# Kernel optimization log

Hardware: AMD Instinct MI355X
Metric: run time of the kernel (lower is better)

## Reference

```python
import math
import jax, jax.numpy as jnp
import numpy as np


def _gelu(x):
    return jax.nn.gelu(x, approximate=False)


def _bilinear_sample(feat, gx, gy):
    """grid_sample, mode=bilinear, padding=border, align_corners=True.
    feat: [B,C,H,W]; gx,gy: [B,M] in [-1,1]. Returns [B,M,C]."""
    B, C, H, W = feat.shape
    x = jnp.clip((gx + 1.0) * 0.5 * (W - 1), 0.0, W - 1)
    y = jnp.clip((gy + 1.0) * 0.5 * (H - 1), 0.0, H - 1)
    x0 = jnp.floor(x); y0 = jnp.floor(y)
    wx = (x - x0)[..., None]; wy = (y - y0)[..., None]
    x0i = x0.astype(jnp.int32); y0i = y0.astype(jnp.int32)
    x1i = jnp.minimum(x0i + 1, W - 1); y1i = jnp.minimum(y0i + 1, H - 1)
    ft = jnp.transpose(feat, (0, 2, 3, 1))  # [B,H,W,C]
    gather = jax.vmap(lambda f, yi, xi: f[yi, xi])
    v00 = gather(ft, y0i, x0i); v01 = gather(ft, y0i, x1i)
    v10 = gather(ft, y1i, x0i); v11 = gather(ft, y1i, x1i)
    return (v00 * (1 - wx) * (1 - wy) + v01 * wx * (1 - wy)
            + v10 * (1 - wx) * wy + v11 * wx * wy)


def _layernorm(x, w, b, eps=1e-5):
    m = jnp.mean(x, -1, keepdims=True)
    v = jnp.var(x, -1, keepdims=True)
    return (x - m) / jnp.sqrt(v + eps) * w + b


def _gfb(h, f_next, ph_w, ph_b, gate, w1, b1, w2, b2, ln_w, ln_b):
    g = jax.nn.sigmoid(gate)
    fused = f_next + g * (h @ ph_w + ph_b)
    fused = _gelu(fused @ w1 + b1) @ w2 + b2
    return _layernorm(fused, ln_w, ln_b)


def _forward(img, feat_s8, feat_s16, coarse_flow, query_coords,
             pp_w1, pp_b1, pp_w2, pp_b2, p8_w, p8_b, p16_w, p16_b,
             f1_ph_w, f1_ph_b, f1_gate, f1_w1, f1_b1, f1_w2, f1_b2, f1_ln_w, f1_ln_b,
             f2_ph_w, f2_ph_b, f2_gate, f2_w1, f2_b1, f2_w2, f2_b2, f2_ln_w, f2_ln_b,
             h_w1, h_b1, h_w2, h_b2, h_w3, h_b3):
    B, _, H, W = img.shape
    N = query_coords.shape[1]
    k = 5; half = k // 2
    H8, W8 = coarse_flow.shape[2], coarse_flow.shape[3]
    # normalized grid at query points (x,y)
    gx = 2.0 * query_coords[..., 0] / (W - 1) - 1.0
    gy = 2.0 * query_coords[..., 1] / (H - 1) - 1.0
    coarse_q = _bilinear_sample(coarse_flow, gx, gy)  # [B,N,2]
    coarse_q = coarse_q * jnp.array([W / W8, H / H8], coarse_q.dtype)
    # local k x k RGB patches
    offs = jnp.arange(-half, half + 1, dtype=img.dtype)
    oy, ox = jnp.meshgrid(offs, offs, indexing='ij')
    og = jnp.stack([ox.reshape(-1), oy.reshape(-1)], -1)  # [k*k,2]
    ce = query_coords[:, :, None, :] + og                # [B,N,kk,2]
    pgx = (2.0 * ce[..., 0] / (W - 1) - 1.0).reshape(B, -1)
    pgy = (2.0 * ce[..., 1] / (H - 1) - 1.0).reshape(B, -1)
    patches = _bilinear_sample(img, pgx, pgy).reshape(B, N, k * k * 3)
    f_local = _gelu(patches @ pp_w1 + pp_b1) @ pp_w2 + pp_b2
    f8 = _bilinear_sample(feat_s8, gx, gy) @ p8_w + p8_b
    f16 = _bilinear_sample(feat_s16, gx, gy) @ p16_w + p16_b
    D = f_local.shape[-1]
    h = f_local.reshape(B * N, D)
    h = _gfb(h, f8.reshape(B * N, D), f1_ph_w, f1_ph_b, f1_gate,
             f1_w1, f1_b1, f1_w2, f1_b2, f1_ln_w, f1_ln_b)
    h = _gfb(h, f16.reshape(B * N, D), f2_ph_w, f2_ph_b, f2_gate,
             f2_w1, f2_b1, f2_w2, f2_b2, f2_ln_w, f2_ln_b)
    # relative-in-cell coords + sinusoidal PE (6 bands)
    qx = query_coords[..., 0] / (W / W8)
    qy = query_coords[..., 1] / (H / H8)
    local = jnp.stack([(qx - jnp.round(qx)) * 2.0, (qy - jnp.round(qy)) * 2.0], -1)
    freqs = (2.0 ** jnp.arange(6, dtype=local.dtype)) * math.pi
    xf = local[..., None] * freqs                        # [B,N,2,6]
    enc = jnp.concatenate([jnp.sin(xf), jnp.cos(xf)], -1).reshape(B, N, 24)
    pe = jnp.concatenate([local, enc], -1).reshape(B * N, 26)
    coarse_flat = coarse_q.reshape(B * N, 2)
    mi = jnp.concatenate([h, pe, coarse_flat], -1)       # [B*N, 156]
    delta = _gelu(_gelu(mi @ h_w1 + h_b1) @ h_w2 + h_b2) @ h_w3 + h_b3
    return (coarse_flat + delta).reshape(B, N, 2)


def setup_inputs() -> dict:
    key = jax.random.key(0)
    ks = jax.random.split(key, 40)
    B, H, W = 2, 384, 512
    H8, W8, H16, W16 = 48, 64, 24, 32
    N, D, k = 65536, 128, 5
    pf = 3 * k * k
    def p(i, shape):
        return jax.random.normal(ks[i], shape, jnp.float32) * 0.05
    return {
        'img': jax.random.uniform(ks[0], (B, 3, H, W), jnp.float32),
        'feat_s8': jax.random.normal(ks[1], (B, D, H8, W8), jnp.float32),
        'feat_s16': jax.random.normal(ks[2], (B, D, H16, W16), jnp.float32),
        'coarse_flow': jax.random.normal(ks[3], (B, 2, H8, W8), jnp.float32),
        'query_coords': jax.random.uniform(ks[4], (B, N, 2), jnp.float32)
                        * jnp.array([W - 1.0, H - 1.0], jnp.float32),
        'pp_w1': p(5, (pf, D)), 'pp_b1': p(6, (D,)),
        'pp_w2': p(7, (D, D)), 'pp_b2': p(8, (D,)),
        'p8_w': p(9, (D, D)), 'p8_b': p(10, (D,)),
        'p16_w': p(11, (D, D)), 'p16_b': p(12, (D,)),
        'f1_ph_w': p(13, (D, D)), 'f1_ph_b': p(14, (D,)), 'f1_gate': p(15, (D,)),
        'f1_w1': p(16, (D, 2 * D)), 'f1_b1': p(17, (2 * D,)),
        'f1_w2': p(18, (2 * D, D)), 'f1_b2': p(19, (D,)),
        'f1_ln_w': 1.0 + p(20, (D,)), 'f1_ln_b': p(21, (D,)),
        'f2_ph_w': p(22, (D, D)), 'f2_ph_b': p(23, (D,)), 'f2_gate': p(24, (D,)),
        'f2_w1': p(25, (D, 2 * D)), 'f2_b1': p(26, (2 * D,)),
        'f2_w2': p(27, (2 * D, D)), 'f2_b2': p(28, (D,)),
        'f2_ln_w': 1.0 + p(29, (D,)), 'f2_ln_b': p(30, (D,)),
        'h_w1': p(31, (D + 26 + 2, 128)), 'h_b1': p(32, (128,)),
        'h_w2': p(33, (128, 64)), 'h_b2': p(34, (64,)),
        'h_w3': p(35, (64, 2)), 'h_b3': p(36, (2,)),
    }


def reference(img, feat_s8, feat_s16, coarse_flow, query_coords,
              pp_w1, pp_b1, pp_w2, pp_b2, p8_w, p8_b, p16_w, p16_b,
              f1_ph_w, f1_ph_b, f1_gate, f1_w1, f1_b1, f1_w2, f1_b2, f1_ln_w, f1_ln_b,
              f2_ph_w, f2_ph_b, f2_gate, f2_w1, f2_b1, f2_w2, f2_b2, f2_ln_w, f2_ln_b,
              h_w1, h_b1, h_w2, h_b2, h_w3, h_b3):
    return _forward(img, feat_s8, feat_s16, coarse_flow, query_coords,
                    pp_w1, pp_b1, pp_w2, pp_b2, p8_w, p8_b, p16_w, p16_b,
                    f1_ph_w, f1_ph_b, f1_gate, f1_w1, f1_b1, f1_w2, f1_b2, f1_ln_w, f1_ln_b,
                    f2_ph_w, f2_ph_b, f2_gate, f2_w1, f2_b1, f2_w2, f2_b2, f2_ln_w, f2_ln_b,
                    h_w1, h_b1, h_w2, h_b2, h_w3, h_b3)
```

## Files before the change

kernel.cpp:

```cpp
#include <hip/hip_runtime.h>
#include <math.h>

#define NT 512
#define MB 64
#define MTOT 131072
#define IMG_H 384
#define IMG_W 512
#define H8 48
#define W8 64
#define H16 24
#define W16 32

#define SAB 128
#define SPE 40

typedef _Float16 half8_t __attribute__((ext_vector_type(8)));
typedef _Float16 half4_t __attribute__((ext_vector_type(4)));
typedef float f32x4_t __attribute__((ext_vector_type(4)));
typedef unsigned short u16;

#define SWZ(r, gi) ((gi) ^ ((r) & 7))

#define PW_PP1    0
#define PW_MEGA1  12288
#define PW_S8     77824
#define PW_MEGA2  110592
#define PW_S15    176128
#define PW_HW1    208896
#define PW_HW2    229376
#define PW_END    237568
#define FT8_OFF   PW_END
#define FT8_CNT   (2*H8*W8*128)
#define FT16_OFF  (FT8_OFF + FT8_CNT)
#define FT16_CNT  (2*H16*W16*128)
#define F32_OFF   (FT16_OFF + FT16_CNT)
#define PEG_OFF   (F32_OFF + 2*164608)
#define PEG_CNT   (2048*MB*SPE)
#define CBG_OFF   (PEG_OFF + PEG_CNT)

__device__ __forceinline__ u16 tohalf(float v) {
  return __builtin_bit_cast(u16, (_Float16)v);
}
__device__ __forceinline__ float geluf(float x) {
  float x2 = x * x;
  float t = x * fmaf(x2, 0.0713548162726f, 1.5957691216057308f);
  float e = __expf(-t);
  return x * __builtin_amdgcn_rcpf(1.0f + e);
}

__device__ __forceinline__ float bilin_plane(const float* __restrict__ plane,
                                             int Wd, int Hd, float x, float y) {
  x = fminf(fmaxf(x, 0.f), (float)(Wd - 1));
  y = fminf(fmaxf(y, 0.f), (float)(Hd - 1));
  float x0f = floorf(x), y0f = floorf(y);
  int x0 = (int)x0f, y0 = (int)y0f;
  int x1 = min(x0 + 1, Wd - 1), y1 = min(y0 + 1, Hd - 1);
  float wx = x - x0f, wy = y - y0f;
  const float* r0 = plane + y0 * Wd;
  const float* r1 = plane + y1 * Wd;
  float v00 = r0[x0], v01 = r0[x1], v10 = r1[x0], v11 = r1[x1];
  float top = v00 + wx * (v01 - v00);
  float bot = v10 + wx * (v11 - v10);
  return top + wy * (bot - top);
}

__device__ __forceinline__ void featSample(const u16* __restrict__ ft, int Wd, int Hd,
                                           float x, float y, u16* dstRow,
                                           int i16, int giS) {
  x = fminf(fmaxf(x, 0.f), (float)(Wd - 1));
  y = fminf(fmaxf(y, 0.f), (float)(Hd - 1));
  float x0f = floorf(x), y0f = floorf(y);
  int x0 = (int)x0f, y0 = (int)y0f;
  int x1 = min(x0 + 1, Wd - 1), y1 = min(y0 + 1, Hd - 1);
  _Float16 wx = (_Float16)(x - x0f), wy = (_Float16)(y - y0f);
  half8_t v00 = *reinterpret_cast<const half8_t*>(ft + (y0 * Wd + x0) * 128 + i16 * 8);
  half8_t v01 = *reinterpret_cast<const half8_t*>(ft + (y0 * Wd + x1) * 128 + i16 * 8);
  half8_t v10 = *reinterpret_cast<const half8_t*>(ft + (y1 * Wd + x0) * 128 + i16 * 8);
  half8_t v11 = *reinterpret_cast<const half8_t*>(ft + (y1 * Wd + x1) * 128 + i16 * 8);
  half8_t top = v00 + wx * (v01 - v00);
  half8_t bot = v10 + wx * (v11 - v10);
  half8_t r = top + wy * (bot - top);
  *reinterpret_cast<half8_t*>(dstRow + giS * 8) = r;
}

template <int KT, int SPLITKT, int ACT, int SWB = 1, int NWAVES = 8>
__device__ __forceinline__ void mmv(
    const u16* __restrict__ wpk,
    const u16* aA, const u16* aB, int strB,
    const float* __restrict__ bias,
    u16* ob) {
  const int tid = threadIdx.x;
  const int lane = tid & 63;
  const int w = tid >> 6;
  const int l15 = lane & 15;
  const int g = lane >> 4;
  if (NWAVES == 8 || w < NWAVES) {
    f32x4_t acc[4];
#pragma unroll
    for (int mt = 0; mt < 4; ++mt) acc[mt] = (f32x4_t){0.f, 0.f, 0.f, 0.f};
    __builtin_amdgcn_s_setprio(1);
#pragma unroll
    for (int kt = 0; kt < KT; ++kt) {
      half8_t af[4];
#pragma unroll
      for (int mt = 0; mt < 4; ++mt) {
        const int row = mt * 16 + l15;
        const u16* p;
        if (kt < SPLITKT) {
          p = aA + row * 128 + SWZ(row, kt * 4 + g) * 8;
        } else if (SWB) {
          p = aB + row * 128 + SWZ(row, (kt - SPLITKT) * 4 + g) * 8;
        } else {
          p = aB + row * strB + (kt - SPLITKT) * 32 + g * 8;
        }
        af[mt] = *reinterpret_cast<const half8_t*>(p);
      }
      half8_t bf = *reinterpret_cast<const half8_t*>(wpk + ((w * KT + kt) * 64 + lane) * 8);
#pragma unroll
      for (int mt = 0; mt < 4; ++mt)
        acc[mt] = __builtin_amdgcn_mfma_f32_16x16x32_f16(bf, af[mt], acc[mt], 0, 0, 0);
    }
    __builtin_amdgcn_s_setprio(0);
    const int c0 = (w << 4) + (g << 2);
    f32x4_t bv = *reinterpret_cast<const f32x4_t*>(bias + c0);
#pragma unroll
    for (int mt = 0; mt < 4; ++mt) {
      const int row = (mt << 4) + l15;
      half4_t hv;
#pragma unroll
      for (int r = 0; r < 4; ++r) {
        float v = acc[mt][r] + bv[r];
        if (ACT == 1) v = geluf(v);
        hv[r] = (_Float16)v;
      }
      const int e = row * 128 + (c0 ^ ((row & 7) << 3));
      *reinterpret_cast<half4_t*>(ob + e) = hv;
    }
  }
}

__device__ __forceinline__ void lnorm(const u16* src, u16* dst,
                                      const float* __restrict__ lw,
                                      const float* __restrict__ lb) {
  const int tid = threadIdx.x;
  int q = tid >> 3, s = tid & 7;
  float xs[16];
  float sum = 0.f, sum2 = 0.f;
#pragma unroll
  for (int c8 = 0; c8 < 2; ++c8) {
    const int gi = SWZ(q, 2 * s + c8);
    half8_t v = *reinterpret_cast<const half8_t*>(src + q * 128 + gi * 8);
#pragma unroll
    for (int j = 0; j < 8; ++j) {
      float x = (float)v[j];
      xs[c8 * 8 + j] = x; sum += x; sum2 += x * x;
    }
  }
  sum += __shfl_xor(sum, 1); sum2 += __shfl_xor(sum2, 1);
  sum += __shfl_xor(sum, 2); sum2 += __shfl_xor(sum2, 2);
  sum += __shfl_xor(sum, 4); sum2 += __shfl_xor(sum2, 4);
  float mean = sum * 0.0078125f;
  float var = sum2 * 0.0078125f - mean * mean;
  float rstd = rsqrtf(var + 1e-5f);
#pragma unroll
  for (int c8 = 0; c8 < 2; ++c8) {
    half8_t r;
#pragma unroll
    for (int j = 0; j < 8; ++j) {
      int c = s * 16 + c8 * 8 + j;
      r[j] = (_Float16)((xs[c8 * 8 + j] - mean) * rstd * lw[c] + lb[c]);
    }
    const int gi = SWZ(q, 2 * s + c8);
    *reinterpret_cast<half8_t*>(dst + q * 128 + gi * 8) = r;
  }
}

struct PrepArgs {
  const float *f1_ph_w, *f1_gate, *f2_ph_w, *f2_gate;
  const float *p8_w, *p16_w, *f1_w1, *f2_w1;
  const float *p8_b, *f1_ph_b, *p16_b, *f2_ph_b, *f2_b1;
  const float *feat8, *feat16;
  float *T1, *WAtop, *WBtop, *WBbot, *bvec1, *bB;
  u16 *ft8, *ft16;
};

__global__ void prepA(PrepArgs a) {
  const int blk = blockIdx.x;
  const int tid = threadIdx.x;
  if (blk < 2056) {
    const int o = tid >> 2, ks = tid & 3;
    float acc = 0.f;
    if (blk < 2048) {
      const int sec = blk >> 9;
      const int oid = (blk & 511) * 64 + o;
      const int r = oid >> 8, n = oid & 255;
#pragma unroll 8
      for (int i = 0; i < 32; ++i) {
        const int m = ks * 32 + i;
        if (sec == 0) {
          float sig = __builtin_amdgcn_rcpf(1.f + __expf(-a.f1_gate[m]));
          acc += sig * a.f1_ph_w[r * 128 + m] * a.f1_w1[m * 256 + n];
        } else if (sec == 1) {
          acc += a.p8_w[r * 128 + m] * a.f1_w1[m * 256 + n];
        } else if (sec == 2) {
          acc += a.p16_w[r * 128 + m] * a.f2_w1[m * 256 + n];
        } else {
          float sig = __builtin_amdgcn_rcpf(1.f + __expf(-a.f2_gate[m]));
          acc += sig * a.f2_ph_w[r * 128 + m] * a.f2_w1[m * 256 + n];
        }
      }
      acc += __shfl_xor(acc, 1);
      acc += __shfl_xor(acc, 2);
      if (ks == 0) {
        float* dst = (sec == 0) ? a.T1 : (sec == 1) ? a.WAtop
                     : (sec == 2) ? a.WBtop : a.WBbot;
        dst[oid] = acc;
      }
    } else {
      const int oid = (blk - 2048) * 64 + o;
#pragma unroll 8
      for (int i = 0; i < 32; ++i) {
        const int m = ks * 32 + i;
        if (oid < 256) {
          float sig = __builtin_amdgcn_rcpf(1.f + __expf(-a.f1_gate[m]));
          acc += (a.p8_b[m] + sig * a.f1_ph_b[m]) * a.f1_w1[m * 256 + oid];
        } else {
          float sig = __builtin_amdgcn_rcpf(1.f + __expf(-a.f2_gate[m]));
          acc += (a.p16_b[m] + sig * a.f2_ph_b[m]) * a.f2_w1[m * 256 + (oid - 256)];
        }
      }
      acc += __shfl_xor(acc, 1);
      acc += __shfl_xor(acc, 2);
      if (ks == 0) {
        if (oid < 256) a.bvec1[oid] = acc;
        else a.bB[oid - 256] = a.f2_b1[oid - 256] + acc;
      }
    }
  } else {
    const int tot8 = 2 * 128 * H8 * W8;
    const int i = (blk - 2056) * 256 + tid;
    if (i < tot8) {
      int x = i % W8;
      int t = i / W8;
      int y = t % H8; t /= H8;
      int c = t % 128;
      int b = t / 128;
      a.ft8[((b * H8 + y) * W8 + x) * 128 + c] = tohalf(a.feat8[i]);
    } else {
      int i2 = i - tot8;
      int x = i2 % W16;
      int t = i2 / W16;
      int y = t % H16; t /= H16;
      int c = t % 128;
      int b = t / 128;
      a.ft16[((b * H16 + y) * W16 + x) * 128 + c] = tohalf(a.feat16[i2]);
    }
  }
}

__global__ void prepB(const float* __restrict__ pp_w2, const float* __restrict__ T1,
                      const float* __restrict__ pp_b2, const float* __restrict__ f1_b1,
                      const float* __restrict__ bvec1,
                      float* __restrict__ WAbot, float* __restrict__ bA) {
  const int blk = blockIdx.x;
  const int tid = threadIdx.x;
  const int o = tid >> 2, ks = tid & 3;
  float acc = 0.f;
  if (blk < 512) {
    const int oid = blk * 64 + o;
    const int k = oid >> 8, n = oid & 255;
#pragma unroll 8
    for (int i = 0; i < 32; ++i) {
      const int r = ks * 32 + i;
      acc += pp_w2[k * 128 + r] * T1[r * 256 + n];
    }
    acc += __shfl_xor(acc, 1);
    acc += __shfl_xor(acc, 2);
    if (ks == 0) WAbot[oid] = acc;
  } else {
    const int n = (blk - 512) * 64 + o;
#pragma unroll 8
    for (int i = 0; i < 32; ++i) {
      const int r = ks * 32 + i;
      acc += pp_b2[r] * T1[r * 256 + n];
    }
    acc += __shfl_xor(acc, 1);
    acc += __shfl_xor(acc, 2);
    if (ks == 0) bA[n] = f1_b1[n] + bvec1[n] + acc;
  }
}

struct PackArgs {
  const float *pp_w1, *f1_w2, *f2_w2, *h_w1, *h_w2;
  const float *WAtop, *WAbot, *WBtop, *WBbot;
  u16* dst;
};

__global__ void pack_weights(PackArgs a) {
  const int KTs[7]   = {3, 8, 8, 8, 8, 5, 4};
  const int Ks[7]    = {75, 256, 256, 256, 256, 156, 128};
  const int bases[8] = {0, 12288, 77824, 110592, 176128, 208896, 229376, 237568};
  int stride = gridDim.x * blockDim.x;
  for (int i = blockIdx.x * blockDim.x + threadIdx.x; i < PW_END; i += stride) {
    int s = 0;
    while (i >= bases[s + 1]) ++s;
    int rem = i - bases[s];
    int e = rem & 511, lane = e >> 3, j = e & 7;
    int ntkt = rem >> 9;
    int kt = ntkt % KTs[s], nt = ntkt / KTs[s];
    int k = kt * 32 + ((lane >> 4) << 3) + j;
    int col = (nt << 4) + (lane & 15);
    float v = 0.f;
    if (k < Ks[s]) {
      switch (s) {
        case 0: v = a.pp_w1[k * 128 + col]; break;
        case 1: v = (k < 128) ? a.WAtop[k * 256 + col]
                              : a.WAbot[(k - 128) * 256 + col]; break;
        case 2: v = a.f1_w2[k * 128 + col]; break;
        case 3: v = (k < 128) ? a.WBtop[k * 256 + col]
                              : a.WBbot[(k - 128) * 256 + col]; break;
        case 4: v = a.f2_w2[k * 128 + col]; break;
        case 5: v = a.h_w1[k * 128 + col]; break;
        case 6: v = a.h_w2[k * 64 + col]; break;
      }
    }
    a.dst[i] = tohalf(v);
  }
}

struct KParams {
  const float *img, *coarse_flow, *qc;
  const u16 *wpk, *ft8, *ft16;
  const float *bA, *bB;
  u16* peg;
  float* cbg;
  const float *pp_b1;
  const float *f1_b2, *f1_ln_w, *f1_ln_b;
  const float *f2_b2, *f2_ln_w, *f2_ln_b;
  const float *h_b1, *h_b2, *h_w3, *h_b3;
  float* out;
};

__global__ __launch_bounds__(NT, 2) void ifd_mfma(KParams P) {
  __shared__ __align__(16) u16 smem[4 * MB * SAB];
  u16* ab0 = smem;
  u16* ab1 = smem + MB * SAB;
  u16* tb  = smem + 2 * MB * SAB;
  u16* hb  = smem + 3 * MB * SAB;

  const int tid = threadIdx.x;
  const int m0 = blockIdx.x * MB;
  u16* pegB = P.peg + blockIdx.x * (MB * SPE);
  float* cbgB = P.cbg + blockIdx.x * (MB * 2);

  {
    const int q = tid >> 3, sub = tid & 7;
    const int m = m0 + q, b = m >> 16;
    const float qx = P.qc[2 * m], qy = P.qc[2 * m + 1];
    const float* imgb = P.img + b * 3 * (IMG_H * IMG_W);
#pragma unroll
    for (int j = 0; j < 12; ++j) {
      const int c = sub * 12 + j;
      u16 val = 0;
      if (c < 75) {
        int p = c / 3, ch = c - p * 3;
        int iy = p / 5, ix = p - iy * 5;
        val = tohalf(bilin_plane(imgb + ch * (IMG_H * IMG_W), IMG_W, IMG_H,
                                 qx + (float)(ix - 2), qy + (float)(iy - 2)));
      }
      ab0[q * 128 + (c ^ ((q & 7) << 3))] = val;
    }
  }
  if (tid < 128) {
    const int q = tid >> 1, dim = tid & 1;
    const int m = m0 + q;
    const float qv = P.qc[2 * m + dim];
    const float q8 = qv * 0.125f;
    const float loc = (q8 - rintf(q8)) * 2.f;
    pegB[q * SPE + dim] = tohalf(loc);
    const float th = loc * 3.14159265358979323846f;
    float s = __sinf(th), c = __cosf(th);
    const int base = q * SPE + 2 + dim * 12;
#pragma unroll
    for (int bnd = 0; bnd < 6; ++bnd) {
      pegB[base + bnd] = tohalf(s);
      pegB[base + 6 + bnd] = tohalf(c);
      float s2 = 2.f * s * c;
      c = fmaf(-2.f * s, s, 1.f);
      s = s2;
    }
  } else if (tid < 256) {
    const int t2 = tid - 128, q = t2 >> 1, o = t2 & 1;
    const int m = m0 + q, b = m >> 16;
    const float qx = P.qc[2 * m], qy = P.qc[2 * m + 1];
    const float x8 = qx * (63.f / 511.f), y8 = qy * (47.f / 383.f);
    const float cv = 8.f * bilin_plane(P.coarse_flow + (b * 2 + o) * (H8 * W8),
                                       W8, H8, x8, y8);
    pegB[q * SPE + 26 + o] = tohalf(cv);
    cbgB[q * 2 + o] = cv;
  } else if (tid < 384) {
    const int t2 = tid - 256, q = t2 >> 1, pr = t2 & 1;
    *reinterpret_cast<unsigned int*>(pegB + q * SPE + 28 + 2 * pr) = 0u;
  }
  __syncthreads();

  mmv<3, 3, 1>(P.wpk + PW_PP1, ab0, ab0, 128, P.pp_b1, ab1);
  for (int i = tid; i < MB * 16; i += NT) {
    int q = i >> 4, i16 = i & 15;
    int m = m0 + q, b = m >> 16;
    float x = P.qc[2 * m] * (63.f / 511.f), y = P.qc[2 * m + 1] * (47.f / 383.f);
    featSample(P.ft8 + b * (H8 * W8 * 128), W8, H8, x, y, hb + q * 128,
               i16, SWZ(q, i16));
  }
  __syncthreads();

  mmv<8, 4, 1>(P.wpk + PW_MEGA1, hb, ab1, 128, P.bA, ab0);
  mmv<8, 4, 1>(P.wpk + PW_MEGA1 + 32768, hb, ab1, 128, P.bA + 128, tb);
  __syncthreads();

  mmv<8, 4, 0>(P.wpk + PW_S8, ab0, tb, 128, P.f1_b2, ab1);
  __syncthreads();

  lnorm(ab1, hb, P.f1_ln_w, P.f1_ln_b);
  for (int i = tid; i < MB * 16; i += NT) {
    int q = i >> 4, i16 = i & 15;
    int m = m0 + q, b = m >> 16;
    float x = P.qc[2 * m] * (31.f / 511.f), y = P.qc[2 * m + 1] * (23.f / 383.f);
    featSample(P.ft16 + b * (H16 * W16 * 128), W16, H16, x, y, ab0 + q * 128,
               i16, SWZ(q, i16));
  }
  __syncthreads();

  mmv<8, 4, 1>(P.wpk + PW_MEGA2, ab0, hb, 128, P.bB, ab1);
  mmv<8, 4, 1>(P.wpk + PW_MEGA2 + 32768, ab0, hb, 128, P.bB + 128, tb);
  __syncthreads();

  mmv<8, 4, 0>(P.wpk + PW_S15, ab1, tb, 128, P.f2_b2, ab0);
  __syncthreads();

  lnorm(ab0, hb, P.f2_ln_w, P.f2_ln_b);
  __syncthreads();

  mmv<5, 4, 1, 0>(P.wpk + PW_HW1, hb, pegB, SPE, P.h_b1, ab1);
  __syncthreads();

  mmv<4, 4, 1, 1, 4>(P.wpk + PW_HW2, ab1, ab1, 128, P.h_b2, ab0);
  __syncthreads();

  if (tid < 2 * MB) {
    int q = tid >> 1, o = tid & 1;
    float acc = P.h_b3[o];
    const u16* rp = ab0 + q * 128;
#pragma unroll
    for (int c8 = 0; c8 < 8; ++c8) {
      half8_t v = *reinterpret_cast<const half8_t*>(rp + SWZ(q, c8) * 8);
#pragma unroll
      for (int j = 0; j < 8; ++j) acc += (float)v[j] * P.h_w3[(c8 * 8 + j) * 2 + o];
    }
    P.out[(m0 + q) * 2 + o] = cbgB[q * 2 + o] + acc;
  }
}

extern "C" void kernel_launch(void* const* d_in, const int* in_sizes, int n_in,
                              void* d_out, int out_size, void* d_ws, size_t ws_size,
                              hipStream_t stream) {
  u16* wp = (u16*)d_ws;
  float* fbase = (float*)(wp + F32_OFF);
  float* T1    = fbase;
  float* WAtop = fbase + 32768;
  float* WAbot = fbase + 65536;
  float* WBtop = fbase + 98304;
  float* WBbot = fbase + 131072;
  float* bvec1 = fbase + 163840;
  float* bA    = fbase + 164096;
  float* bB    = fbase + 164352;
  u16* peg = wp + PEG_OFF;
  float* cbg = (float*)(wp + CBG_OFF);

  PrepArgs pra;
  pra.f1_ph_w = (const float*)d_in[13];
  pra.f1_gate = (const float*)d_in[15];
  pra.f2_ph_w = (const float*)d_in[22];
  pra.f2_gate = (const float*)d_in[24];
  pra.p8_w = (const float*)d_in[9];
  pra.p16_w = (const float*)d_in[11];
  pra.f1_w1 = (const float*)d_in[16];
  pra.f2_w1 = (const float*)d_in[25];
  pra.p8_b = (const float*)d_in[10];
  pra.f1_ph_b = (const float*)d_in[14];
  pra.p16_b = (const float*)d_in[12];
  pra.f2_ph_b = (const float*)d_in[23];
  pra.f2_b1 = (const float*)d_in[26];
  pra.feat8 = (const float*)d_in[1];
  pra.feat16 = (const float*)d_in[2];
  pra.T1 = T1; pra.WAtop = WAtop; pra.WBtop = WBtop; pra.WBbot = WBbot;
  pra.bvec1 = bvec1; pra.bB = bB;
  pra.ft8 = wp + FT8_OFF; pra.ft16 = wp + FT16_OFF;
  prepA<<<2056 + 3840, 256, 0, stream>>>(pra);

  prepB<<<516, 256, 0, stream>>>((const float*)d_in[7], T1, (const float*)d_in[8],
                                 (const float*)d_in[17], bvec1, WAbot, bA);

  PackArgs pa;
  pa.pp_w1 = (const float*)d_in[5];
  pa.f1_w2 = (const float*)d_in[18];
  pa.f2_w2 = (const float*)d_in[27];
  pa.h_w1  = (const float*)d_in[31];
  pa.h_w2  = (const float*)d_in[33];
  pa.WAtop = WAtop; pa.WAbot = WAbot; pa.WBtop = WBtop; pa.WBbot = WBbot;
  pa.dst = wp;
  pack_weights<<<464, 256, 0, stream>>>(pa);

  KParams P;
  P.img = (const float*)d_in[0];
  P.coarse_flow = (const float*)d_in[3];
  P.qc = (const float*)d_in[4];
  P.wpk = wp; P.ft8 = wp + FT8_OFF; P.ft16 = wp + FT16_OFF;
  P.bA = bA; P.bB = bB;
  P.peg = peg; P.cbg = cbg;
  P.pp_b1 = (const float*)d_in[6];
  P.f1_b2 = (const float*)d_in[19];
  P.f1_ln_w = (const float*)d_in[20]; P.f1_ln_b = (const float*)d_in[21];
  P.f2_b2 = (const float*)d_in[28];
  P.f2_ln_w = (const float*)d_in[29]; P.f2_ln_b = (const float*)d_in[30];
  P.h_b1 = (const float*)d_in[32]; P.h_b2 = (const float*)d_in[34];
  P.h_w3 = (const float*)d_in[35]; P.h_b3 = (const float*)d_in[36];
  P.out = (float*)d_out;

  ifd_mfma<<<MTOT / MB, NT, 0, stream>>>(P);
}
```

Measured before the change: 196.5 us.

## Merge three weight-prep kernels into one prep_all launch with reassociated products

Replaces the prepA, prepB and pack_weights launches with a single prep_all kernel. Each block builds one row of the folded weight matrix in LDS, multiplies it by W1 and writes the packed fp16 MFMA layout directly, so the fp32 intermediates T1/WA/WB are no longer stored and reloaded. The pp_w2·f1_ph_w product is reassociated so it is computed per row before multiplying by W1. This removes two launches and their global round trips. The cost is serial 128-long dot products per thread with low parallelism in the row blocks.

```diff
diff --git a/kernel.cpp b/kernel.cpp
--- a/kernel.cpp
+++ b/kernel.cpp
@@ -34,7 +34,7 @@
 #define FT16_OFF  (FT8_OFF + FT8_CNT)
 #define FT16_CNT  (2*H16*W16*128)
 #define F32_OFF   (FT16_OFF + FT16_CNT)
-#define PEG_OFF   (F32_OFF + 2*164608)
+#define PEG_OFF   (F32_OFF + 2*512)
 #define PEG_CNT   (2048*MB*SPE)
 #define CBG_OFF   (PEG_OFF + PEG_CNT)
 
@@ -175,70 +175,97 @@
   }
 }
 
-struct PrepArgs {
-  const float *f1_ph_w, *f1_gate, *f2_ph_w, *f2_gate;
-  const float *p8_w, *p16_w, *f1_w1, *f2_w1;
-  const float *p8_b, *f1_ph_b, *p16_b, *f2_ph_b, *f2_b1;
+struct PrepAllArgs {
+  const float *pp_w1, *pp_w2, *p8_w, *p16_w, *f1_ph_w, *f1_gate, *f1_w1, *f1_w2;
+  const float *f2_ph_w, *f2_gate, *f2_w1, *f2_w2, *h_w1, *h_w2;
+  const float *p8_b, *f1_ph_b, *pp_b2, *f1_b1, *p16_b, *f2_ph_b, *f2_b1;
   const float *feat8, *feat16;
-  float *T1, *WAtop, *WBtop, *WBbot, *bvec1, *bB;
+  u16 *dst;
+  float *bA, *bB;
   u16 *ft8, *ft16;
 };
 
-__global__ void prepA(PrepArgs a) {
+__global__ void prep_all(PrepAllArgs a) {
+  __shared__ float lds[256];
   const int blk = blockIdx.x;
   const int tid = threadIdx.x;
-  if (blk < 2056) {
-    const int o = tid >> 2, ks = tid & 3;
-    float acc = 0.f;
-    if (blk < 2048) {
-      const int sec = blk >> 9;
-      const int oid = (blk & 511) * 64 + o;
-      const int r = oid >> 8, n = oid & 255;
-#pragma unroll 8
-      for (int i = 0; i < 32; ++i) {
-        const int m = ks * 32 + i;
-        if (sec == 0) {
-          float sig = __builtin_amdgcn_rcpf(1.f + __expf(-a.f1_gate[m]));
-          acc += sig * a.f1_ph_w[r * 128 + m] * a.f1_w1[m * 256 + n];
-        } else if (sec == 1) {
-          acc += a.p8_w[r * 128 + m] * a.f1_w1[m * 256 + n];
-        } else if (sec == 2) {
-          acc += a.p16_w[r * 128 + m] * a.f2_w1[m * 256 + n];
-        } else {
-          float sig = __builtin_amdgcn_rcpf(1.f + __expf(-a.f2_gate[m]));
-          acc += sig * a.f2_ph_w[r * 128 + m] * a.f2_w1[m * 256 + n];
+  if (blk < 512) {
+    const int sec = blk >> 8;
+    const int k = blk & 255;
+    float* Arow = lds;
+    if (sec == 0) {
+      if (k < 128) {
+        if (tid < 128) Arow[tid] = a.p8_w[k * 128 + tid];
+      } else {
+        float* prow = lds + 128;
+        if (tid < 128) prow[tid] = a.pp_w2[(k - 128) * 128 + tid];
+        __syncthreads();
+        if (tid < 128) {
+          float sig = __builtin_amdgcn_rcpf(1.f + __expf(-a.f1_gate[tid]));
+          float acc = 0.f;
+          for (int r = 0; r < 128; ++r) acc += prow[r] * a.f1_ph_w[r * 128 + tid];
+          Arow[tid] = acc * sig;
         }
       }
-      acc += __shfl_xor(acc, 1);
-      acc += __shfl_xor(acc, 2);
-      if (ks == 0) {
-        float* dst = (sec == 0) ? a.T1 : (sec == 1) ? a.WAtop
-                     : (sec == 2) ? a.WBtop : a.WBbot;
-        dst[oid] = acc;
-      }
     } else {
-      const int oid = (blk - 2048) * 64 + o;
-#pragma unroll 8
-      for (int i = 0; i < 32; ++i) {
-        const int m = ks * 32 + i;
-        if (oid < 256) {
-          float sig = __builtin_amdgcn_rcpf(1.f + __expf(-a.f1_gate[m]));
-          acc += (a.p8_b[m] + sig * a.f1_ph_b[m]) * a.f1_w1[m * 256 + oid];
-        } else {
-          float sig = __builtin_amdgcn_rcpf(1.f + __expf(-a.f2_gate[m]));
-          acc += (a.p16_b[m] + sig * a.f2_ph_b[m]) * a.f2_w1[m * 256 + (oid - 256)];
+      if (k < 128) {
+        if (tid < 128) Arow[tid] = a.p16_w[k * 128 + tid];
+      } else {
+        if (tid < 128) {
+          float sig = __builtin_amdgcn_rcpf(1.f + __expf(-a.f2_gate[tid]));
+          Arow[tid] = a.f2_ph_w[(k - 128) * 128 + tid] * sig;
         }
       }
-      acc += __shfl_xor(acc, 1);
-      acc += __shfl_xor(acc, 2);
-      if (ks == 0) {
-        if (oid < 256) a.bvec1[oid] = acc;
-        else a.bB[oid - 256] = a.f2_b1[oid - 256] + acc;
-      }
-    }
+    }
+    __syncthreads();
+    const float* W1 = (sec == 0) ? a.f1_w1 : a.f2_w1;
+    float acc = 0.f;
+    for (int m = 0; m < 128; ++m) acc += Arow[m] * W1[m * 256 + tid];
+    const int kt = k >> 5, hi = (k >> 3) & 3, j = k & 7;
+    const int nt = tid >> 4, lo = tid & 15;
+    const int base = (sec == 0) ? PW_MEGA1 : PW_MEGA2;
+    a.dst[base + (((nt * 8 + kt) * 64 + hi * 16 + lo) << 3) + j] = tohalf(acc);
+  } else if (blk == 512) {
+    float* u = lds;
+    if (tid < 128) {
+      float sig = __builtin_amdgcn_rcpf(1.f + __expf(-a.f1_gate[tid]));
+      float acc = 0.f;
+      for (int r = 0; r < 128; ++r) acc += a.pp_b2[r] * a.f1_ph_w[r * 128 + tid];
+      u[tid] = a.p8_b[tid] + sig * a.f1_ph_b[tid] + sig * acc;
+    }
+    __syncthreads();
+    float acc = a.f1_b1[tid];
+    for (int m = 0; m < 128; ++m) acc += u[m] * a.f1_w1[m * 256 + tid];
+    a.bA[tid] = acc;
+  } else if (blk == 513) {
+    float acc = a.f2_b1[tid];
+    for (int m = 0; m < 128; ++m) {
+      float sig = __builtin_amdgcn_rcpf(1.f + __expf(-a.f2_gate[m]));
+      acc += (a.p16_b[m] + sig * a.f2_ph_b[m]) * a.f2_w1[m * 256 + tid];
+    }
+    a.bB[tid] = acc;
+  } else if (blk < 930) {
+    const int vi = (blk - 514) * 256 + tid;
+    const int vb[6] = {0, 12288, 45056, 77824, 98304, 106496};
+    const int KTs[5] = {3, 8, 8, 5, 4};
+    const int Ks[5]  = {75, 256, 256, 156, 128};
+    const int Ns[5]  = {128, 128, 128, 128, 64};
+    const int pw[5]  = {PW_PP1, PW_S8, PW_S15, PW_HW1, PW_HW2};
+    int s = 0;
+    while (vi >= vb[s + 1]) ++s;
+    const int rem = vi - vb[s];
+    const int e = rem & 511, lane = e >> 3, j = e & 7;
+    const int ntkt = rem >> 9;
+    const int kt = ntkt % KTs[s], nt = ntkt / KTs[s];
+    const int k = kt * 32 + ((lane >> 4) << 3) + j;
+    const int col = (nt << 4) + (lane & 15);
+    const float* src = (s == 0) ? a.pp_w1 : (s == 1) ? a.f1_w2
+                     : (s == 2) ? a.f2_w2 : (s == 3) ? a.h_w1 : a.h_w2;
+    float v = (k < Ks[s]) ? src[k * Ns[s] + col] : 0.f;
+    a.dst[pw[s] + rem] = tohalf(v);
   } else {
     const int tot8 = 2 * 128 * H8 * W8;
-    const int i = (blk - 2056) * 256 + tid;
+    const int i = (blk - 930) * 256 + tid;
     if (i < tot8) {
       int x = i % W8;
       int t = i / W8;
@@ -258,76 +285,6 @@
   }
 }
 
-__global__ void prepB(const float* __restrict__ pp_w2, const float* __restrict__ T1,
-                      const float* __restrict__ pp_b2, const float* __restrict__ f1_b1,
-                      const float* __restrict__ bvec1,
-                      float* __restrict__ WAbot, float* __restrict__ bA) {
-  const int blk = blockIdx.x;
-  const int tid = threadIdx.x;
-  const int o = tid >> 2, ks = tid & 3;
-  float acc = 0.f;
-  if (blk < 512) {
-    const int oid = blk * 64 + o;
-    const int k = oid >> 8, n = oid & 255;
-#pragma unroll 8
-    for (int i = 0; i < 32; ++i) {
-      const int r = ks * 32 + i;
-      acc += pp_w2[k * 128 + r] * T1[r * 256 + n];
-    }
-    acc += __shfl_xor(acc, 1);
-    acc += __shfl_xor(acc, 2);
-    if (ks == 0) WAbot[oid] = acc;
-  } else {
-    const int n = (blk - 512) * 64 + o;
-#pragma unroll 8
-    for (int i = 0; i < 32; ++i) {
-      const int r = ks * 32 + i;
-      acc += pp_b2[r] * T1[r * 256 + n];
-    }
-    acc += __shfl_xor(acc, 1);
-    acc += __shfl_xor(acc, 2);
-    if (ks == 0) bA[n] = f1_b1[n] + bvec1[n] + acc;
-  }
-}
-
-struct PackArgs {
-  const float *pp_w1, *f1_w2, *f2_w2, *h_w1, *h_w2;
-  const float *WAtop, *WAbot, *WBtop, *WBbot;
-  u16* dst;
-};
-
-__global__ void pack_weights(PackArgs a) {
-  const int KTs[7]   = {3, 8, 8, 8, 8, 5, 4};
-  const int Ks[7]    = {75, 256, 256, 256, 256, 156, 128};
-  const int bases[8] = {0, 12288, 77824, 110592, 176128, 208896, 229376, 237568};
-  int stride = gridDim.x * blockDim.x;
-  for (int i = blockIdx.x * blockDim.x + threadIdx.x; i < PW_END; i += stride) {
-    int s = 0;
-    while (i >= bases[s + 1]) ++s;
-    int rem = i - bases[s];
-    int e = rem & 511, lane = e >> 3, j = e & 7;
-    int ntkt = rem >> 9;
-    int kt = ntkt % KTs[s], nt = ntkt / KTs[s];
-    int k = kt * 32 + ((lane >> 4) << 3) + j;
-    int col = (nt << 4) + (lane & 15);
-    float v = 0.f;
-    if (k < Ks[s]) {
-      switch (s) {
-        case 0: v = a.pp_w1[k * 128 + col]; break;
-        case 1: v = (k < 128) ? a.WAtop[k * 256 + col]
-                              : a.WAbot[(k - 128) * 256 + col]; break;
-        case 2: v = a.f1_w2[k * 128 + col]; break;
-        case 3: v = (k < 128) ? a.WBtop[k * 256 + col]
-                              : a.WBbot[(k - 128) * 256 + col]; break;
-        case 4: v = a.f2_w2[k * 128 + col]; break;
-        case 5: v = a.h_w1[k * 128 + col]; break;
-        case 6: v = a.h_w2[k * 64 + col]; break;
-      }
-    }
-    a.dst[i] = tohalf(v);
-  }
-}
-
 struct KParams {
   const float *img, *coarse_flow, *qc;
   const u16 *wpk, *ft8, *ft16;
@@ -466,50 +423,40 @@
                               hipStream_t stream) {
   u16* wp = (u16*)d_ws;
   float* fbase = (float*)(wp + F32_OFF);
-  float* T1    = fbase;
-  float* WAtop = fbase + 32768;
-  float* WAbot = fbase + 65536;
-  float* WBtop = fbase + 98304;
-  float* WBbot = fbase + 131072;
-  float* bvec1 = fbase + 163840;
-  float* bA    = fbase + 164096;
-  float* bB    = fbase + 164352;
+  float* bA = fbase;
+  float* bB = fbase + 256;
   u16* peg = wp + PEG_OFF;
   float* cbg = (float*)(wp + CBG_OFF);
 
-  PrepArgs pra;
+  PrepAllArgs pra;
+  pra.pp_w1 = (const float*)d_in[5];
+  pra.pp_w2 = (const float*)d_in[7];
+  pra.p8_w  = (const float*)d_in[9];
+  pra.p16_w = (const float*)d_in[11];
   pra.f1_ph_w = (const float*)d_in[13];
   pra.f1_gate = (const float*)d_in[15];
+  pra.f1_w1 = (const float*)d_in[16];
+  pra.f1_w2 = (const float*)d_in[18];
   pra.f2_ph_w = (const float*)d_in[22];
   pra.f2_gate = (const float*)d_in[24];
-  pra.p8_w = (const float*)d_in[9];
-  pra.p16_w = (const float*)d_in[11];
-  pra.f1_w1 = (const float*)d_in[16];
   pra.f2_w1 = (const float*)d_in[25];
-  pra.p8_b = (const float*)d_in[10];
+  pra.f2_w2 = (const float*)d_in[27];
+  pra.h_w1  = (const float*)d_in[31];
+  pra.h_w2  = (const float*)d_in[33];
+  pra.p8_b  = (const float*)d_in[10];
   pra.f1_ph_b = (const float*)d_in[14];
+  pra.pp_b2 = (const float*)d_in[8];
+  pra.f1_b1 = (const float*)d_in[17];
   pra.p16_b = (const float*)d_in[12];
   pra.f2_ph_b = (const float*)d_in[23];
   pra.f2_b1 = (const float*)d_in[26];
   pra.feat8 = (const float*)d_in[1];
   pra.feat16 = (const float*)d_in[2];
-  pra.T1 = T1; pra.WAtop = WAtop; pra.WBtop = WBtop; pra.WBbot = WBbot;
-  pra.bvec1 = bvec1; pra.bB = bB;
-  pra.ft8 = wp + FT8_OFF; pra.ft16 = wp + FT16_OFF;
-  prepA<<<2056 + 3840, 256, 0, stream>>>(pra);
-
-  prepB<<<516, 256, 0, stream>>>((const float*)d_in[7], T1, (const float*)d_in[8],
-                                 (const float*)d_in[17], bvec1, WAbot, bA);
-
-  PackArgs pa;
-  pa.pp_w1 = (const float*)d_in[5];
-  pa.f1_w2 = (const float*)d_in[18];
-  pa.f2_w2 = (const float*)d_in[27];
-  pa.h_w1  = (const float*)d_in[31];
-  pa.h_w2  = (const float*)d_in[33];
-  pa.WAtop = WAtop; pa.WAbot = WAbot; pa.WBtop = WBtop; pa.WBbot = WBbot;
-  pa.dst = wp;
-  pack_weights<<<464, 256, 0, stream>>>(pa);
+  pra.dst = wp;
+  pra.bA = bA; pra.bB = bB;
+  pra.ft8 = wp + FT8_OFF;
+  pra.ft16 = wp + FT16_OFF;
+  prep_all<<<4770, 256, 0, stream>>>(pra);
 
   KParams P;
   P.img = (const float*)d_in[0];
```

Measured after the change: 169.1 us (median of 2 runs). 1.16x faster.
